# Performance work log

Hardware: AMD Instinct MI355X
Metric: run time of the kernel (lower is better)

## Reference

```python
import jax, jax.numpy as jnp
import numpy as np

DIM = 192
HEADS = 6
WS = 7          # window size
SHIFT = 3       # shift size
HID = 768       # mlp hidden
EPS = 1e-5


def _rel_pos_index(ws):
    coords = np.stack(np.meshgrid(np.arange(ws), np.arange(ws), indexing='ij'))  # (2, ws, ws)
    cf = coords.reshape(2, -1)                       # (2, ws*ws)
    rel = cf[:, :, None] - cf[:, None, :]            # (2, N, N)
    rel = rel.transpose(1, 2, 0).astype(np.int64)
    rel[:, :, 0] += ws - 1
    rel[:, :, 1] += ws - 1
    rel[:, :, 0] *= 2 * ws - 1
    return jnp.asarray(rel.sum(-1))                  # (N, N)

REL_IDX = _rel_pos_index(WS)


def _layernorm(x, w, b):
    mu = jnp.mean(x, axis=-1, keepdims=True)
    var = jnp.mean(jnp.square(x - mu), axis=-1, keepdims=True)
    return (x - mu) * jax.lax.rsqrt(var + EPS) * w + b


def setup_inputs() -> dict:
    key = jax.random.key(0)
    ks = jax.random.split(key, 8)
    B, H, W = 32, 56, 56
    s = 0.02
    return {
        'x': jax.random.normal(ks[0], (B, H * W, DIM), jnp.float32),
        'norm1_w': jnp.ones((DIM,), jnp.float32),
        'norm1_b': jnp.zeros((DIM,), jnp.float32),
        'qkv_w': jax.random.normal(ks[1], (3 * DIM, DIM), jnp.float32) * s,
        'qkv_b': jnp.zeros((3 * DIM,), jnp.float32),
        'rpb_table': jax.random.normal(ks[2], ((2 * WS - 1) ** 2, HEADS), jnp.float32) * s,
        'proj_w': jax.random.normal(ks[3], (DIM, DIM), jnp.float32) * s,
        'proj_b': jnp.zeros((DIM,), jnp.float32),
        'norm2_w': jnp.ones((DIM,), jnp.float32),
        'norm2_b': jnp.zeros((DIM,), jnp.float32),
        'fc1_w': jax.random.normal(ks[4], (HID, DIM), jnp.float32) * s,
        'fc1_b': jnp.zeros((HID,), jnp.float32),
        'fc2_w': jax.random.normal(ks[5], (DIM, HID), jnp.float32) * s,
        'fc2_b': jnp.zeros((DIM,), jnp.float32),
        'H': H,
        'W': W,
    }


def reference(x, norm1_w, norm1_b, qkv_w, qkv_b, rpb_table, proj_w, proj_b,
              norm2_w, norm2_b, fc1_w, fc1_b, fc2_w, fc2_b, H, W):
    B, L, C = x.shape
    d = C // HEADS
    scale = d ** -0.5
    N = WS * WS

    shortcut = x
    h = _layernorm(x, norm1_w, norm1_b).reshape(B, H, W, C)
    if SHIFT > 0:
        h = jnp.roll(h, shift=(-SHIFT, -SHIFT), axis=(1, 2))

    # window partition -> (B * nW, N, C)
    h = h.reshape(B, H // WS, WS, W // WS, WS, C).transpose(0, 1, 3, 2, 4, 5)
    hw = h.reshape(-1, N, C)

    # windowed attention (NOTE: the torch block never passes a shift mask)
    qkv = hw @ qkv_w.T + qkv_b                                    # (B_, N, 3C)
    qkv = qkv.reshape(-1, N, 3, HEADS, d).transpose(2, 0, 3, 1, 4)
    q, k, v = qkv[0] * scale, qkv[1], qkv[2]                      # (B_, h, N, d)
    attn = jnp.einsum('bhnd,bhmd->bhnm', q, k)
    bias = rpb_table[REL_IDX].transpose(2, 0, 1)                  # (h, N, N)
    attn = jax.nn.softmax(attn + bias[None], axis=-1)
    out = jnp.einsum('bhnm,bhmd->bhnd', attn, v)
    out = out.transpose(0, 2, 1, 3).reshape(-1, N, C)
    out = out @ proj_w.T + proj_b

    # window reverse -> (B, H, W, C)
    out = out.reshape(B, H // WS, W // WS, WS, WS, C).transpose(0, 1, 3, 2, 4, 5)
    out = out.reshape(B, H, W, C)
    if SHIFT > 0:
        out = jnp.roll(out, shift=(SHIFT, SHIFT), axis=(1, 2))

    x = shortcut + out.reshape(B, L, C)
    h2 = _layernorm(x, norm2_w, norm2_b)
    mlp = jax.nn.gelu(h2 @ fc1_w.T + fc1_b, approximate=False) @ fc2_w.T + fc2_b
    return x + mlp
```

## Files before the change

### kernel.cpp

```cpp
#include <hip/hip_runtime.h>
#include <hip/hip_bf16.h>
#include <cmath>

typedef float f32x4 __attribute__((ext_vector_type(4)));
typedef __bf16 bf16x8 __attribute__((ext_vector_type(8)));
typedef __bf16 bf16x4 __attribute__((ext_vector_type(4)));

#define WS_SZ 7
#define SHIFT 3
#define HGRID 56
#define C_DIM 192
#define NHEADS 6
#define HDIM 32
#define NTOK 100352
#define NWIN 2048

__device__ __forceinline__ int win_to_tok(int wrow) {
    int w = wrow / 49, i = wrow - w * 49;
    int b = w >> 6, rem = w & 63;
    int wy = rem >> 3, wx = rem & 7;
    int yi = i / 7, xi = i - yi * 7;
    int y = wy * 7 + yi + SHIFT; if (y >= HGRID) y -= HGRID;
    int x = wx * 7 + xi + SHIFT; if (x >= HGRID) x -= HGRID;
    return b * (HGRID * HGRID) + y * HGRID + x;
}

__global__ __launch_bounds__(256)
void cvt_kernel(const float* __restrict__ src, __bf16* __restrict__ dst, int n8)
{
    int idx = blockIdx.x * 256 + threadIdx.x;
    if (idx >= n8) return;
    float4 a = ((const float4*)src)[idx * 2];
    float4 b = ((const float4*)src)[idx * 2 + 1];
    bf16x8 o;
    o[0] = (__bf16)a.x; o[1] = (__bf16)a.y; o[2] = (__bf16)a.z; o[3] = (__bf16)a.w;
    o[4] = (__bf16)b.x; o[5] = (__bf16)b.y; o[6] = (__bf16)b.z; o[7] = (__bf16)b.w;
    ((bf16x8*)dst)[idx] = o;
}

__global__ __launch_bounds__(256)
void bias_expand_kernel(const float* __restrict__ rpb, float* __restrict__ bias_g)
{
    int idx = blockIdx.x * 256 + threadIdx.x;
    if (idx >= NHEADS * 2401) return;
    int h = idx / 2401, rem = idx - h * 2401;
    int i = rem / 49, j = rem - i * 49;
    int yi = i / 7, xi = i - yi * 7;
    int yj = j / 7, xj = j - yj * 7;
    int ri = (yi - yj + 6) * 13 + (xi - xj + 6);
    bias_g[idx] = rpb[ri * NHEADS + h];
}

template<int WINDOWED>
__global__ __launch_bounds__(256)
void ln_kernel(const float* __restrict__ x, const float* __restrict__ w,
               const float* __restrict__ b, __bf16* __restrict__ out)
{
    int r = blockIdx.x * 4 + (threadIdx.x >> 6);
    int lane = threadIdx.x & 63;
    int src = WINDOWED ? win_to_tok(r) : r;
    const float* xp = x + (size_t)src * C_DIM;
    float v0 = xp[lane], v1 = xp[lane + 64], v2 = xp[lane + 128];
    float s = v0 + v1 + v2;
    float sq = v0 * v0 + v1 * v1 + v2 * v2;
    #pragma unroll
    for (int off = 32; off; off >>= 1) {
        s  += __shfl_xor(s, off);
        sq += __shfl_xor(sq, off);
    }
    float mu = s * (1.f / C_DIM);
    float rs = rsqrtf(sq * (1.f / C_DIM) - mu * mu + 1e-5f);
    __bf16* op = out + (size_t)r * C_DIM;
    op[lane]       = (__bf16)((v0 - mu) * rs * w[lane]       + b[lane]);
    op[lane + 64]  = (__bf16)((v1 - mu) * rs * w[lane + 64]  + b[lane + 64]);
    op[lane + 128] = (__bf16)((v2 - mu) * rs * w[lane + 128] + b[lane + 128]);
}

template<int MODE>
__global__ __launch_bounds__(256)
void gemm_kernel(const __bf16* __restrict__ A, const __bf16* __restrict__ W,
                 const float* __restrict__ bias, void* __restrict__ outp,
                 const float* __restrict__ resid, int N, int K)
{
    __shared__ __bf16 As[128 * 40];
    __shared__ __bf16 Bs[64 * 40];
    const int tid = threadIdx.x;
    const int wave = tid >> 6, lane = tid & 63;
    const int wm = wave >> 1, wn = wave & 1;
    const int l15 = lane & 15, q8 = (lane >> 4) << 3;
    const int m0 = blockIdx.y * 128, n0 = blockIdx.x * 64;

    f32x4 acc[4][2];
    f32x4 zero = {0.f, 0.f, 0.f, 0.f};
    #pragma unroll
    for (int i = 0; i < 4; i++)
        #pragma unroll
        for (int j = 0; j < 2; j++) acc[i][j] = zero;

    const int br = tid >> 2, bc = (tid & 3) << 3;
    for (int kt = 0; kt < K; kt += 32) {
        __syncthreads();
        #pragma unroll
        for (int it = 0; it < 2; it++) {
            int idx = it * 256 + tid;
            int r = idx >> 2, c = (idx & 3) << 3;
            *(uint4*)(&As[r * 40 + c]) =
                *(const uint4*)(A + (size_t)(m0 + r) * K + kt + c);
        }
        *(uint4*)(&Bs[br * 40 + bc]) =
            *(const uint4*)(W + (size_t)(n0 + br) * K + kt + bc);
        __syncthreads();
        bf16x8 af[4], bfr[2];
        #pragma unroll
        for (int fm = 0; fm < 4; fm++)
            af[fm] = *(const bf16x8*)(&As[(wm * 64 + fm * 16 + l15) * 40 + q8]);
        #pragma unroll
        for (int fn = 0; fn < 2; fn++)
            bfr[fn] = *(const bf16x8*)(&Bs[(wn * 32 + fn * 16 + l15) * 40 + q8]);
        #pragma unroll
        for (int fm = 0; fm < 4; fm++)
            #pragma unroll
            for (int fn = 0; fn < 2; fn++)
                acc[fm][fn] = __builtin_amdgcn_mfma_f32_16x16x32_bf16(
                    af[fm], bfr[fn], acc[fm][fn], 0, 0, 0);
    }

    const int l4 = lane >> 4;
    #pragma unroll
    for (int fm = 0; fm < 4; fm++) {
        #pragma unroll
        for (int fn = 0; fn < 2; fn++) {
            int c = n0 + wn * 32 + fn * 16 + l15;
            float bv = bias[c];
            #pragma unroll
            for (int r = 0; r < 4; r++) {
                int m = m0 + wm * 64 + fm * 16 + l4 * 4 + r;
                float v = acc[fm][fn][r] + bv;
                if (MODE == 0) {
                    ((__bf16*)outp)[(size_t)m * N + c] = (__bf16)v;
                } else {
                    int t = win_to_tok(m);
                    ((float*)outp)[(size_t)t * C_DIM + c] =
                        resid[(size_t)t * C_DIM + c] + v;
                }
            }
        }
    }
}

__global__ __launch_bounds__(256, 3)
void mlp_fused_kernel(const float* __restrict__ n2w, const float* __restrict__ n2b,
                      const __bf16* __restrict__ w1,
                      const float* __restrict__ b1,
                      const __bf16* __restrict__ w2,
                      const float* __restrict__ b2,
                      float* __restrict__ out)
{
    __shared__ __align__(16) __bf16 As[64 * 200];
    __shared__ __bf16 Hs[64 * 72];
    const int tid = threadIdx.x;
    const int wn = tid >> 6, lane = tid & 63;
    const int l15 = lane & 15, q4 = lane >> 4, q8 = q4 << 3;
    const int m0 = blockIdx.x * 64;
    const int r0 = wn * 16;

    const __bf16* w1base = w1 + (size_t)(wn * 16 + l15) * 192 + q8;
    const __bf16* w2base = w2 + (size_t)(wn * 48 + l15) * 768 + q8;

    f32x4 zero = {0.f, 0.f, 0.f, 0.f};

    bf16x8 w1f[2][6];
    #pragma unroll
    for (int kt = 0; kt < 6; ++kt)
        w1f[0][kt] = *(const bf16x8*)(w1base + kt * 32);

    float bv1s[12];
    #pragma unroll
    for (int ch = 0; ch < 12; ++ch)
        bv1s[ch] = b1[ch * 64 + wn * 16 + l15];
    float bv2s[3];
    #pragma unroll
    for (int tn = 0; tn < 3; ++tn)
        bv2s[tn] = b2[wn * 48 + tn * 16 + l15];

    {
        const float wl0 = n2w[lane], wl1 = n2w[lane + 64], wl2 = n2w[lane + 128];
        const float bl0 = n2b[lane], bl1 = n2b[lane + 64], bl2 = n2b[lane + 128];
        #pragma unroll
        for (int rr = 0; rr < 16; ++rr) {
            const float* xp = out + (size_t)(m0 + r0 + rr) * C_DIM;
            float v0 = xp[lane], v1 = xp[lane + 64], v2 = xp[lane + 128];
            float s = v0 + v1 + v2;
            float sq = v0 * v0 + v1 * v1 + v2 * v2;
            #pragma unroll
            for (int off = 32; off; off >>= 1) {
                s  += __shfl_xor(s, off);
                sq += __shfl_xor(sq, off);
            }
            float mu = s * (1.f / C_DIM);
            float rs = rsqrtf(sq * (1.f / C_DIM) - mu * mu + 1e-5f);
            As[(r0 + rr) * 200 + lane]       = (__bf16)((v0 - mu) * rs * wl0 + bl0);
            As[(r0 + rr) * 200 + lane + 64]  = (__bf16)((v1 - mu) * rs * wl1 + bl1);
            As[(r0 + rr) * 200 + lane + 128] = (__bf16)((v2 - mu) * rs * wl2 + bl2);
        }
    }
    __syncthreads();

    f32x4 acc2[4][3];
    #pragma unroll
    for (int tm = 0; tm < 4; ++tm)
        #pragma unroll
        for (int tn = 0; tn < 3; ++tn) acc2[tm][tn] = zero;

    bf16x8 w2f[6];

    #pragma unroll
    for (int ch = 0; ch < 12; ++ch) {
        const int h0 = ch * 64;
        const int cur = ch & 1, nxt = cur ^ 1;

        if (ch < 11) {
            #pragma unroll
            for (int kt = 0; kt < 6; ++kt)
                w1f[nxt][kt] = *(const bf16x8*)(w1base + (size_t)(h0 + 64) * 192 + kt * 32);
        }
        #pragma unroll
        for (int ks = 0; ks < 2; ++ks)
            #pragma unroll
            for (int tn = 0; tn < 3; ++tn)
                w2f[ks * 3 + tn] = *(const bf16x8*)(w2base + (size_t)(tn * 16) * 768 + h0 + ks * 32);

        f32x4 acc1[4];
        #pragma unroll
        for (int tm = 0; tm < 4; ++tm) acc1[tm] = zero;
        #pragma unroll
        for (int kt = 0; kt < 6; ++kt)
            #pragma unroll
            for (int tm = 0; tm < 4; ++tm) {
                bf16x8 af = *(const bf16x8*)(&As[(tm * 16 + l15) * 200 + kt * 32 + q8]);
                acc1[tm] = __builtin_amdgcn_mfma_f32_16x16x32_bf16(
                    af, w1f[cur][kt], acc1[tm], 0, 0, 0);
            }

        __syncthreads();

        {
            const float bv = bv1s[ch];
            #pragma unroll
            for (int tm = 0; tm < 4; ++tm)
                #pragma unroll
                for (int r = 0; r < 4; ++r) {
                    int row = tm * 16 + q4 * 4 + r;
                    float v = acc1[tm][r] + bv;
                    float g = v * __builtin_amdgcn_rcpf(1.f + __expf(-1.702f * v));
                    Hs[row * 72 + wn * 16 + l15] = (__bf16)g;
                }
        }
        __syncthreads();

        #pragma unroll
        for (int ks = 0; ks < 2; ++ks)
            #pragma unroll
            for (int tm = 0; tm < 4; ++tm) {
                bf16x8 ap = *(const bf16x8*)(&Hs[(tm * 16 + l15) * 72 + ks * 32 + q8]);
                #pragma unroll
                for (int tn = 0; tn < 3; ++tn)
                    acc2[tm][tn] = __builtin_amdgcn_mfma_f32_16x16x32_bf16(
                        ap, w2f[ks * 3 + tn], acc2[tm][tn], 0, 0, 0);
            }
    }

    float* Cs = (float*)As;
    #pragma unroll
    for (int pass = 0; pass < 2; ++pass) {
        if (pass) __syncthreads();
        #pragma unroll
        for (int tmh = 0; tmh < 2; ++tmh) {
            int tm = pass * 2 + tmh;
            #pragma unroll
            for (int tn = 0; tn < 3; ++tn) {
                int c = wn * 48 + tn * 16 + l15;
                float bv = bv2s[tn];
                #pragma unroll
                for (int r = 0; r < 4; ++r) {
                    int rl = tmh * 16 + q4 * 4 + r;
                    Cs[rl * 196 + c] = acc2[tm][tn][r] + bv;
                }
            }
        }
        __syncthreads();
        #pragma unroll
        for (int it = 0; it < 6; ++it) {
            int f = it * 256 + tid;
            int row = f / 48, c4 = f - row * 48;
            float4* gp = (float4*)(out + (size_t)(m0 + pass * 32 + row) * C_DIM) + c4;
            float4 g = *gp;
            const float* lp = &Cs[row * 196 + c4 * 4];
            g.x += lp[0]; g.y += lp[1]; g.z += lp[2]; g.w += lp[3];
            *gp = g;
        }
    }
}

__global__ __launch_bounds__(64)
void attn_mfma_kernel(const __bf16* __restrict__ qkv,
                      const float* __restrict__ bias_g,
                      __bf16* __restrict__ out)
{
    const int lane = threadIdx.x & 63;
    const int pair = blockIdx.x;
    const int w = pair / 6, head = pair - (pair / 6) * 6;

    __shared__ __bf16 vsT[32 * 72];
    __shared__ __bf16 Ps[64 * 72];

    const int l15 = lane & 15, q4 = lane >> 4, q8 = q4 << 3;
    const size_t qbase = (size_t)w * 49 * 576 + head * 32;

    bf16x8 qf[4], kf[4];
    #pragma unroll
    for (int t = 0; t < 4; ++t) {
        int row = t * 16 + l15;
        int rq = row < 49 ? row : 48;
        qf[t] = *(const bf16x8*)(qkv + qbase + (size_t)rq * 576 + q8);
        kf[t] = *(const bf16x8*)(qkv + qbase + (size_t)rq * 576 + 192 + q8);
    }

    {
        int j0 = lane >> 2, dq = (lane & 3) << 3;
        #pragma unroll
        for (int p = 0; p < 4; ++p) {
            int j = p * 16 + j0;
            if (j < 49) {
                bf16x8 vv = *(const bf16x8*)(qkv + qbase + (size_t)j * 576 + 384 + dq);
                #pragma unroll
                for (int e = 0; e < 8; ++e)
                    vsT[(dq + e) * 72 + j] = vv[e];
            }
        }
        for (int idx = lane; idx < 32 * 15; idx += 64) {
            int dd = idx / 15, jj = 49 + (idx - dd * 15);
            vsT[dd * 72 + jj] = (__bf16)0.f;
        }
    }

    f32x4 sc[4][4];
    f32x4 zero = {0.f, 0.f, 0.f, 0.f};
    #pragma unroll
    for (int tn = 0; tn < 4; ++tn)
        #pragma unroll
        for (int tm = 0; tm < 4; ++tm) sc[tn][tm] = zero;
    __builtin_amdgcn_s_setprio(1);
    #pragma unroll
    for (int tn = 0; tn < 4; ++tn)
        #pragma unroll
        for (int tm = 0; tm < 4; ++tm)
            sc[tn][tm] = __builtin_amdgcn_mfma_f32_16x16x32_bf16(
                kf[tn], qf[tm], sc[tn][tm], 0, 0, 0);
    __builtin_amdgcn_s_setprio(0);

    const float scale = 0.17677669529663687f;
    const int hbase = head * 2401;
    const int jb4 = q4 * 4;
    #pragma unroll
    for (int tm = 0; tm < 4; ++tm) {
        int i = tm * 16 + l15;
        int ioff = hbase + (i < 49 ? i : 48) * 49;
        float v[4][4];
        #pragma unroll
        for (int tn = 0; tn < 4; ++tn) {
            int jb = tn * 16 + jb4;
            #pragma unroll
            for (int r = 0; r < 4; ++r) {
                int j = jb + r;
                float bz = (j < 49) ? bias_g[ioff + j] : 0.f;
                float t = sc[tn][tm][r] * scale + bz;
                v[tn][r] = (j < 49) ? t : -1e30f;
            }
        }
        float mx = v[0][0];
        #pragma unroll
        for (int tn = 0; tn < 4; ++tn)
            #pragma unroll
            for (int r = 0; r < 4; ++r) mx = fmaxf(mx, v[tn][r]);
        mx = fmaxf(mx, __shfl_xor(mx, 16));
        mx = fmaxf(mx, __shfl_xor(mx, 32));
        float sm = 0.f;
        #pragma unroll
        for (int tn = 0; tn < 4; ++tn)
            #pragma unroll
            for (int r = 0; r < 4; ++r) {
                float e = __expf(v[tn][r] - mx);
                v[tn][r] = e;
                sm += e;
            }
        sm += __shfl_xor(sm, 16);
        sm += __shfl_xor(sm, 32);
        float inv = __builtin_amdgcn_rcpf(sm);
        if (i < 49) {
            #pragma unroll
            for (int tn = 0; tn < 4; ++tn) {
                int jb = tn * 16 + jb4;
                bf16x4 pk;
                #pragma unroll
                for (int r = 0; r < 4; ++r)
                    pk[r] = (__bf16)((jb + r < 49) ? v[tn][r] * inv : 0.f);
                *(bf16x4*)(&Ps[i * 72 + jb]) = pk;
            }
        }
    }


    f32x4 oc[4][2];
    #pragma unroll
    for (int tm = 0; tm < 4; ++tm)
        #pragma unroll
        for (int tn = 0; tn < 2; ++tn) oc[tm][tn] = zero;
    #pragma unroll
    for (int ks = 0; ks < 2; ++ks) {
        bf16x8 bv[2];
        #pragma unroll
        for (int tn = 0; tn < 2; ++tn)
            bv[tn] = *(const bf16x8*)(vsT + (tn * 16 + l15) * 72 + ks * 32 + q8);
        __builtin_amdgcn_s_setprio(1);
        #pragma unroll
        for (int tm = 0; tm < 4; ++tm) {
            bf16x8 ap = *(const bf16x8*)(Ps + (tm * 16 + l15) * 72 + ks * 32 + q8);
            #pragma unroll
            for (int tn = 0; tn < 2; ++tn)
                oc[tm][tn] = __builtin_amdgcn_mfma_f32_16x16x32_bf16(
                    ap, bv[tn], oc[tm][tn], 0, 0, 0);
        }
        __builtin_amdgcn_s_setprio(0);
    }

    #pragma unroll
    for (int tm = 0; tm < 4; ++tm) {
        #pragma unroll
        for (int r = 0; r < 4; ++r) {
            int m = tm * 16 + q4 * 4 + r;
            if (m < 49) {
                __bf16* op = out + (size_t)(w * 49 + m) * C_DIM + head * 32;
                #pragma unroll
                for (int tn = 0; tn < 2; ++tn)
                    op[tn * 16 + l15] = (__bf16)(oc[tm][tn][r]);
            }
        }
    }
}

extern "C" void kernel_launch(void* const* d_in, const int* in_sizes, int n_in,
                              void* d_out, int out_size, void* d_ws, size_t ws_size,
                              hipStream_t stream) {
    const float* x     = (const float*)d_in[0];
    const float* n1w   = (const float*)d_in[1];
    const float* n1b   = (const float*)d_in[2];
    const float* qkvw  = (const float*)d_in[3];
    const float* qkvb  = (const float*)d_in[4];
    const float* rpb   = (const float*)d_in[5];
    const float* projw = (const float*)d_in[6];
    const float* projb = (const float*)d_in[7];
    const float* n2w   = (const float*)d_in[8];
    const float* n2b   = (const float*)d_in[9];
    const float* fc1w  = (const float*)d_in[10];
    const float* fc1b  = (const float*)d_in[11];
    const float* fc2w  = (const float*)d_in[12];
    const float* fc2b  = (const float*)d_in[13];
    float* out = (float*)d_out;
    char* ws = (char*)d_ws;

    __bf16* bufA    = (__bf16*)ws;
    __bf16* bufQ    = (__bf16*)(ws + 38535168);
    __bf16* qkvw_b  = (__bf16*)(ws + 154140672);
    __bf16* projw_b = (__bf16*)(ws + 154361856);
    __bf16* fc1w_b  = (__bf16*)(ws + 154435584);
    __bf16* fc2w_b  = (__bf16*)(ws + 154730496);
    float*  bias_g  = (float*) (ws + 155025408);

    cvt_kernel<<<(110592/8 + 255)/256, 256, 0, stream>>>(qkvw, qkvw_b, 110592/8);
    cvt_kernel<<<(36864/8  + 255)/256, 256, 0, stream>>>(projw, projw_b, 36864/8);
    cvt_kernel<<<(147456/8 + 255)/256, 256, 0, stream>>>(fc1w, fc1w_b, 147456/8);
    cvt_kernel<<<(147456/8 + 255)/256, 256, 0, stream>>>(fc2w, fc2w_b, 147456/8);
    bias_expand_kernel<<<(NHEADS*2401 + 255)/256, 256, 0, stream>>>(rpb, bias_g);

    ln_kernel<1><<<NTOK / 4, 256, 0, stream>>>(x, n1w, n1b, bufA);
    gemm_kernel<0><<<dim3(9, NTOK / 128), 256, 0, stream>>>(
        bufA, qkvw_b, qkvb, bufQ, nullptr, 576, 192);
    attn_mfma_kernel<<<NWIN * NHEADS, 64, 0, stream>>>(bufQ, bias_g, bufA);
    gemm_kernel<1><<<dim3(3, NTOK / 128), 256, 0, stream>>>(
        bufA, projw_b, projb, (void*)out, x, 192, 192);
    mlp_fused_kernel<<<NTOK / 64, 256, 0, stream>>>(
        n2w, n2b, fc1w_b, fc1b, fc2w_b, fc2b, out);
}
```

Baseline: 463.5 us.

## Fuse projection GEMM with residual add and LayerNorm2, merge weight conversions

Replaces the projection GEMM with a kernel that computes full 192-wide rows per block, adds the residual, writes the fp32 result, and computes LayerNorm2 into a bf16 buffer. The MLP kernel then loads precomputed bf16 normalized rows instead of recomputing LayerNorm from fp32. The four weight-conversion launches are merged into one. This removes the MLP kernel's fp32 re-read and scattered residual writes but adds a bf16 intermediate write/read and reloads projection weights per K-tile.

```diff
diff --git a/kernel.cpp b/kernel.cpp
--- a/kernel.cpp
+++ b/kernel.cpp
@@ -26,16 +26,24 @@
 }
 
 __global__ __launch_bounds__(256)
-void cvt_kernel(const float* __restrict__ src, __bf16* __restrict__ dst, int n8)
+void cvt_all_kernel(const float* __restrict__ qkvw, const float* __restrict__ projw,
+                    const float* __restrict__ fc1w, const float* __restrict__ fc2w,
+                    __bf16* __restrict__ qkvw_b, __bf16* __restrict__ projw_b,
+                    __bf16* __restrict__ fc1w_b, __bf16* __restrict__ fc2w_b)
 {
     int idx = blockIdx.x * 256 + threadIdx.x;
-    if (idx >= n8) return;
-    float4 a = ((const float4*)src)[idx * 2];
-    float4 b = ((const float4*)src)[idx * 2 + 1];
+    if (idx >= 55296) return;
+    const float* src; __bf16* dst; int off;
+    if (idx < 13824)      { src = qkvw;  dst = qkvw_b;  off = idx; }
+    else if (idx < 18432) { src = projw; dst = projw_b; off = idx - 13824; }
+    else if (idx < 36864) { src = fc1w;  dst = fc1w_b;  off = idx - 18432; }
+    else                  { src = fc2w;  dst = fc2w_b;  off = idx - 36864; }
+    float4 a = ((const float4*)src)[off * 2];
+    float4 b = ((const float4*)src)[off * 2 + 1];
     bf16x8 o;
     o[0] = (__bf16)a.x; o[1] = (__bf16)a.y; o[2] = (__bf16)a.z; o[3] = (__bf16)a.w;
     o[4] = (__bf16)b.x; o[5] = (__bf16)b.y; o[6] = (__bf16)b.z; o[7] = (__bf16)b.w;
-    ((bf16x8*)dst)[idx] = o;
+    ((bf16x8*)dst)[off] = o;
 }
 
 __global__ __launch_bounds__(256)
@@ -76,11 +84,10 @@
     op[lane + 128] = (__bf16)((v2 - mu) * rs * w[lane + 128] + b[lane + 128]);
 }
 
-template<int MODE>
 __global__ __launch_bounds__(256)
 void gemm_kernel(const __bf16* __restrict__ A, const __bf16* __restrict__ W,
-                 const float* __restrict__ bias, void* __restrict__ outp,
-                 const float* __restrict__ resid, int N, int K)
+                 const float* __restrict__ bias, __bf16* __restrict__ outp,
+                 int N, int K)
 {
     __shared__ __bf16 As[128 * 40];
     __shared__ __bf16 Bs[64 * 40];
@@ -135,21 +142,119 @@
             #pragma unroll
             for (int r = 0; r < 4; r++) {
                 int m = m0 + wm * 64 + fm * 16 + l4 * 4 + r;
-                float v = acc[fm][fn][r] + bv;
-                if (MODE == 0) {
-                    ((__bf16*)outp)[(size_t)m * N + c] = (__bf16)v;
-                } else {
-                    int t = win_to_tok(m);
-                    ((float*)outp)[(size_t)t * C_DIM + c] =
-                        resid[(size_t)t * C_DIM + c] + v;
-                }
+                outp[(size_t)m * N + c] = (__bf16)(acc[fm][fn][r] + bv);
             }
         }
     }
 }
 
 __global__ __launch_bounds__(256, 3)
-void mlp_fused_kernel(const float* __restrict__ n2w, const float* __restrict__ n2b,
+void proj_ln_kernel(const __bf16* __restrict__ A,
+                    const __bf16* __restrict__ W,
+                    const float* __restrict__ pb,
+                    const float* __restrict__ x,
+                    const float* __restrict__ n2w, const float* __restrict__ n2b,
+                    float* __restrict__ out,
+                    __bf16* __restrict__ lnout)
+{
+    __shared__ __align__(16) __bf16 As[64 * 200];
+    __shared__ __bf16 Bs[192 * 40];
+    const int tid = threadIdx.x;
+    const int wn = tid >> 6, lane = tid & 63;
+    const int l15 = lane & 15, q4 = lane >> 4, q8 = q4 << 3;
+    const int m0 = blockIdx.x * 64;
+
+    float bvp[12];
+    #pragma unroll
+    for (int tn = 0; tn < 12; ++tn) bvp[tn] = pb[tn * 16 + l15];
+
+    #pragma unroll
+    for (int it = 0; it < 6; ++it) {
+        int idx = it * 256 + tid;
+        int r = idx / 24, c = (idx - r * 24) << 3;
+        *(uint4*)(&As[r * 200 + c]) =
+            *(const uint4*)(A + (size_t)(m0 + r) * 192 + c);
+    }
+
+    f32x4 zero = {0.f, 0.f, 0.f, 0.f};
+    f32x4 acc[12];
+    #pragma unroll
+    for (int tn = 0; tn < 12; ++tn) acc[tn] = zero;
+
+    const int br = tid >> 2, bc = (tid & 3) << 3;
+    for (int kt = 0; kt < 6; ++kt) {
+        __syncthreads();
+        #pragma unroll
+        for (int it = 0; it < 3; ++it) {
+            int r = br + it * 64;
+            int idx = it * 256 + tid;
+            int rr = idx >> 2, cc = (idx & 3) << 3;
+            *(uint4*)(&Bs[rr * 40 + cc]) =
+                *(const uint4*)(W + (size_t)rr * 192 + kt * 32 + cc);
+        }
+        __syncthreads();
+        bf16x8 af = *(const bf16x8*)(&As[(wn * 16 + l15) * 200 + kt * 32 + q8]);
+        #pragma unroll
+        for (int tn = 0; tn < 12; ++tn) {
+            bf16x8 bfr = *(const bf16x8*)(&Bs[(tn * 16 + l15) * 40 + q8]);
+            acc[tn] = __builtin_amdgcn_mfma_f32_16x16x32_bf16(af, bfr, acc[tn], 0, 0, 0);
+        }
+    }
+
+    float* Cs = (float*)As;
+    const int rowt = tid >> 3, lane8 = tid & 7;
+    const int c0 = lane8 * 24;
+    #pragma unroll
+    for (int pass = 0; pass < 2; ++pass) {
+        __syncthreads();
+        if ((wn >> 1) == pass) {
+            int rl0 = (wn & 1) * 16 + q4 * 4;
+            #pragma unroll
+            for (int tn = 0; tn < 12; ++tn) {
+                int c = tn * 16 + l15;
+                #pragma unroll
+                for (int r = 0; r < 4; ++r)
+                    Cs[(rl0 + r) * 196 + c] = acc[tn][r] + bvp[tn];
+            }
+        }
+        __syncthreads();
+        int m = m0 + pass * 32 + rowt;
+        int t = win_to_tok(m);
+        const float* xp = x + (size_t)t * C_DIM + c0;
+        float* op = out + (size_t)t * C_DIM + c0;
+        float v[24];
+        float s = 0.f, sq = 0.f;
+        #pragma unroll
+        for (int e = 0; e < 24; ++e) {
+            float o = xp[e] + Cs[rowt * 196 + c0 + e];
+            v[e] = o;
+            s += o; sq += o * o;
+        }
+        #pragma unroll
+        for (int e4 = 0; e4 < 6; ++e4) {
+            float4 g = { v[e4*4], v[e4*4+1], v[e4*4+2], v[e4*4+3] };
+            *(float4*)(op + e4 * 4) = g;
+        }
+        s  += __shfl_xor(s, 1);  s  += __shfl_xor(s, 2);  s  += __shfl_xor(s, 4);
+        sq += __shfl_xor(sq, 1); sq += __shfl_xor(sq, 2); sq += __shfl_xor(sq, 4);
+        float mu = s * (1.f / C_DIM);
+        float rs = rsqrtf(sq * (1.f / C_DIM) - mu * mu + 1e-5f);
+        __bf16* lp = lnout + (size_t)t * C_DIM + c0;
+        #pragma unroll
+        for (int e8 = 0; e8 < 3; ++e8) {
+            bf16x8 ob;
+            #pragma unroll
+            for (int e = 0; e < 8; ++e) {
+                int c = c0 + e8 * 8 + e;
+                ob[e] = (__bf16)((v[e8*8+e] - mu) * rs * n2w[c] + n2b[c]);
+            }
+            *(bf16x8*)(lp + e8 * 8) = ob;
+        }
+    }
+}
+
+__global__ __launch_bounds__(256, 3)
+void mlp_fused_kernel(const __bf16* __restrict__ lnA,
                       const __bf16* __restrict__ w1,
                       const float* __restrict__ b1,
                       const __bf16* __restrict__ w2,
@@ -162,7 +267,6 @@
     const int wn = tid >> 6, lane = tid & 63;
     const int l15 = lane & 15, q4 = lane >> 4, q8 = q4 << 3;
     const int m0 = blockIdx.x * 64;
-    const int r0 = wn * 16;
 
     const __bf16* w1base = w1 + (size_t)(wn * 16 + l15) * 192 + q8;
     const __bf16* w2base = w2 + (size_t)(wn * 48 + l15) * 768 + q8;
@@ -183,26 +287,12 @@
     for (int tn = 0; tn < 3; ++tn)
         bv2s[tn] = b2[wn * 48 + tn * 16 + l15];
 
-    {
-        const float wl0 = n2w[lane], wl1 = n2w[lane + 64], wl2 = n2w[lane + 128];
-        const float bl0 = n2b[lane], bl1 = n2b[lane + 64], bl2 = n2b[lane + 128];
-        #pragma unroll
-        for (int rr = 0; rr < 16; ++rr) {
-            const float* xp = out + (size_t)(m0 + r0 + rr) * C_DIM;
-            float v0 = xp[lane], v1 = xp[lane + 64], v2 = xp[lane + 128];
-            float s = v0 + v1 + v2;
-            float sq = v0 * v0 + v1 * v1 + v2 * v2;
-            #pragma unroll
-            for (int off = 32; off; off >>= 1) {
-                s  += __shfl_xor(s, off);
-                sq += __shfl_xor(sq, off);
-            }
-            float mu = s * (1.f / C_DIM);
-            float rs = rsqrtf(sq * (1.f / C_DIM) - mu * mu + 1e-5f);
-            As[(r0 + rr) * 200 + lane]       = (__bf16)((v0 - mu) * rs * wl0 + bl0);
-            As[(r0 + rr) * 200 + lane + 64]  = (__bf16)((v1 - mu) * rs * wl1 + bl1);
-            As[(r0 + rr) * 200 + lane + 128] = (__bf16)((v2 - mu) * rs * wl2 + bl2);
-        }
+    #pragma unroll
+    for (int it = 0; it < 6; ++it) {
+        int idx = it * 256 + tid;
+        int r = idx / 24, c = (idx - r * 24) << 3;
+        *(uint4*)(&As[r * 200 + c]) =
+            *(const uint4*)(lnA + (size_t)(m0 + r) * 192 + c);
     }
     __syncthreads();
 
@@ -409,7 +499,6 @@
             }
         }
     }
-
 
     f32x4 oc[4][2];
     #pragma unroll
@@ -471,24 +560,23 @@
 
     __bf16* bufA    = (__bf16*)ws;
     __bf16* bufQ    = (__bf16*)(ws + 38535168);
+    __bf16* lnout   = bufQ;
     __bf16* qkvw_b  = (__bf16*)(ws + 154140672);
     __bf16* projw_b = (__bf16*)(ws + 154361856);
     __bf16* fc1w_b  = (__bf16*)(ws + 154435584);
     __bf16* fc2w_b  = (__bf16*)(ws + 154730496);
     float*  bias_g  = (float*) (ws + 155025408);
 
-    cvt_kernel<<<(110592/8 + 255)/256, 256, 0, stream>>>(qkvw, qkvw_b, 110592/8);
-    cvt_kernel<<<(36864/8  + 255)/256, 256, 0, stream>>>(projw, projw_b, 36864/8);
-    cvt_kernel<<<(147456/8 + 255)/256, 256, 0, stream>>>(fc1w, fc1w_b, 147456/8);
-    cvt_kernel<<<(147456/8 + 255)/256, 256, 0, stream>>>(fc2w, fc2w_b, 147456/8);
+    cvt_all_kernel<<<216, 256, 0, stream>>>(qkvw, projw, fc1w, fc2w,
+                                            qkvw_b, projw_b, fc1w_b, fc2w_b);
     bias_expand_kernel<<<(NHEADS*2401 + 255)/256, 256, 0, stream>>>(rpb, bias_g);
 
     ln_kernel<1><<<NTOK / 4, 256, 0, stream>>>(x, n1w, n1b, bufA);
-    gemm_kernel<0><<<dim3(9, NTOK / 128), 256, 0, stream>>>(
-        bufA, qkvw_b, qkvb, bufQ, nullptr, 576, 192);
+    gemm_kernel<<<dim3(9, NTOK / 128), 256, 0, stream>>>(
+        bufA, qkvw_b, qkvb, bufQ, 576, 192);
     attn_mfma_kernel<<<NWIN * NHEADS, 64, 0, stream>>>(bufQ, bias_g, bufA);
-    gemm_kernel<1><<<dim3(3, NTOK / 128), 256, 0, stream>>>(
-        bufA, projw_b, projb, (void*)out, x, 192, 192);
+    proj_ln_kernel<<<NTOK / 64, 256, 0, stream>>>(
+        bufA, projw_b, projb, x, n2w, n2b, out, lnout);
     mlp_fused_kernel<<<NTOK / 64, 256, 0, stream>>>(
-        n2w, n2b, fc1w_b, fc1b, fc2w_b, fc2b, out);
-}
+        lnout, fc1w_b, fc1b, fc2w_b, fc2b, out);
+}
```

New measurement: 464.1 us. Within noise of the previous version (+0.1%).
